# Performance work log

Measured on AMD Instinct MI355X. Metric: run time of the kernel, lower is better.

## Reference

```python
import jax, jax.numpy as jnp
import numpy as np

NFRAME = 256
NHOP = 128
BANDS = [0, 4, 8, 12, 16, 20, 24, 28, 32, 40, 44, 48, 52, 56, 64, 72, 80, 88, 96, 104, 112, 128]
NBANDS = 22


def _constants():
    F_bins = NFRAME // 2 + 1
    # sqrt-hann (periodic) analysis window
    n = np.arange(NFRAME)
    win = np.sqrt(0.5 * (1.0 - np.cos(2.0 * np.pi * n / NFRAME))).astype(np.float32)
    # triangular band filterbank matrix [NBANDS, F_bins]
    W = np.zeros((NBANDS, F_bins), np.float32)
    s, e = BANDS[0], BANDS[1]
    W[0, s:e] = 2.0 * (1.0 - np.arange(0, 1, 1.0 / (e - s)))
    s, e = BANDS[-2], BANDS[-1]
    W[-1, s:e] = 2.0 * np.arange(0, 1, 1.0 / (e - s))
    for i, (m, s, e) in enumerate(zip(BANDS[1:-1], BANDS[:-2], BANDS[2:])):
        W[i + 1, s:m] = np.arange(0, 1, 1.0 / (m - s))
        W[i + 1, m:e] = 1.0 - np.arange(0, 1, 1.0 / (e - m))
    # DCT-II matrix [NBANDS, NBANDS]
    nn = np.arange(NBANDS)
    kk = nn[:, None]
    dct = np.cos(np.pi / NBANDS * (nn + 0.5) * kk)
    dct[0] *= 1.0 / np.sqrt(2.0)
    dct *= np.sqrt(2.0 / NBANDS)
    return win, W, dct.astype(np.float32)


def setup_inputs() -> dict:
    key = jax.random.key(0)
    x = jax.random.normal(key, (32, 960000), dtype=jnp.float32)
    return {"x": x}


def reference(x):
    win, W, dct = _constants()
    B, L = x.shape
    chunks = x.reshape(B, L // NHOP, NHOP)
    frames = jnp.concatenate([chunks[:, :-1], chunks[:, 1:]], axis=-1)  # B,T,NFRAME
    frames = frames * jnp.asarray(win)
    spec = jnp.fft.rfft(frames, axis=-1)                # B,T,F complex
    pw = spec.real ** 2 + spec.imag ** 2                # |X|^2 = xk.pow(2).sum(1)
    bands_pow = jnp.einsum('btf,kf->btk', pw, jnp.asarray(W))  # fused filterbank
    feat = jnp.log10(bands_pow) @ jnp.asarray(dct).T    # B,T,22
    return feat
```

## Files before the change

### kernel.cpp

```cpp
#include <hip/hip_runtime.h>

#define NB 22
#define NFR_B 7499
#define BATCH 32
#define ROWLEN 960000
#define NFTOT (BATCH * NFR_B)

typedef float f2 __attribute__((ext_vector_type(2)));

__constant__ int c_bands[NB] = {0,4,8,12,16,20,24,28,32,40,44,48,52,56,64,72,80,88,96,104,112,128};

#define XDPP(x, CTRL) __int_as_float(__builtin_amdgcn_update_dpp(0, __float_as_int(x), CTRL, 0xF, 0xF, true))
#define XSWZ(x, PATT) __int_as_float(__builtin_amdgcn_ds_swizzle(__float_as_int(x), PATT))
#define E0S(x) XDPP(x, 0xB1)
#define E1S(x) XDPP(x, 0x4E)
#define E2S(x) XSWZ(x, 0x101F)
#define E3S(x) XDPP(x, 0x128)
#define E4S(x) XSWZ(x, 0x401F)
#define E5S(x) __shfl_xor(x, 32, 64)

__device__ __forceinline__ f2 mk2(float v) { f2 r; r.x = v; r.y = v; return r; }
__device__ __forceinline__ f2 ex0v(f2 v) { f2 r; r.x = E0S(v.x); r.y = E0S(v.y); return r; }
__device__ __forceinline__ f2 ex1v(f2 v) { f2 r; r.x = E1S(v.x); r.y = E1S(v.y); return r; }
__device__ __forceinline__ f2 ex2v(f2 v) { f2 r; r.x = E2S(v.x); r.y = E2S(v.y); return r; }
__device__ __forceinline__ f2 ex3v(f2 v) { f2 r; r.x = E3S(v.x); r.y = E3S(v.y); return r; }
__device__ __forceinline__ f2 ex4v(f2 v) { f2 r; r.x = E4S(v.x); r.y = E4S(v.y); return r; }
__device__ __forceinline__ f2 ex5v(f2 v) { f2 r; r.x = E5S(v.x); r.y = E5S(v.y); return r; }
__device__ __forceinline__ f2 shflv(f2 v, int idx) {
    f2 r; r.x = __shfl(v.x, idx, 64); r.y = __shfl(v.y, idx, 64); return r;
}

#define PSTAGE(S, EXF)                                                    \
  { const f2 exr_a = EXF(ar2), exi_a = EXF(ai2);                          \
    const f2 exr_b = EXF(br2), exi_b = EXF(bi2);                          \
    const f2 w1r = W1r[S], w1i = W1i[S], w2r = W2r[S], w2i = W2i[S];      \
    const f2 nar = w1r*ar2 - w1i*ai2 + w2r*exr_a - w2i*exi_a;             \
    const f2 nai = w1r*ai2 + w1i*ar2 + w2r*exi_a + w2i*exr_a;             \
    const f2 nbr = w1r*br2 - w1i*bi2 + w2r*exr_b - w2i*exi_b;             \
    const f2 nbi = w1r*bi2 + w1i*br2 + w2r*exi_b + w2i*exr_b;             \
    ar2 = nar; ai2 = nai; br2 = nbr; bi2 = nbi; }

__global__ __launch_bounds__(256, 3)
void feat_kernel(const float* __restrict__ x, float* __restrict__ out) {
    const int lane = threadIdx.x & 63;
    const int wid  = threadIdx.x >> 6;
    const int gwave  = blockIdx.x * (blockDim.x >> 6) + wid;
    const int nwaves = gridDim.x * (blockDim.x >> 6);

    const float PI = 3.14159265358979323846f;

    const int r = (int)(__brev((unsigned)lane) >> 25);

    float winv[4];
    #pragma unroll
    for (int j = 0; j < 4; ++j) winv[j] = sinf(PI * (float)(2 * r + j) / 256.0f);

    f2 W1r[6], W1i[6], W2r[6], W2i[6];
    #pragma unroll
    for (int s = 1; s < 6; ++s) {
        const int m = 1 << s;
        const float ang = -PI * (float)(lane & (m - 1)) / (float)m;
        const float wr = cosf(ang), wi = sinf(ang);
        const bool up = ((lane >> s) & 1) != 0;
        W1r[s] = mk2(up ? -wr : 1.0f);
        W1i[s] = mk2(up ? -wi : 0.0f);
        W2r[s] = mk2(up ? 1.0f : wr);
        W2i[s] = mk2(up ? 0.0f : wi);
    }
    const f2 sgn2 = mk2((lane & 1) ? -1.0f : 1.0f);
    const f2 w6r2 = mk2(cosf(-PI * (float)lane / 64.0f));
    const f2 w6i2 = mk2(sinf(-PI * (float)lane / 64.0f));
    const f2 c1_2 = mk2(cosf(PI * (float)lane / 128.0f));
    const f2 s1_2 = mk2(sinf(PI * (float)lane / 128.0f));

    int seg1 = 0;
    for (int j = 1; j < 14; ++j) if (lane >= c_bands[j]) seg1 = j;
    const int wd1 = c_bands[seg1 + 1] - c_bands[seg1];
    const f2 a1_2 = mk2((float)(lane - c_bands[seg1]) / (float)wd1);
    const f2 m8_2 = mk2((wd1 == 8) ? 1.0f : 0.0f);
    const int bin2 = lane + 64;
    int seg2 = 14;
    for (int j = 15; j < 21; ++j) if (bin2 >= c_bands[j]) seg2 = j;
    const int wd2 = c_bands[seg2 + 1] - c_bands[seg2];
    const f2 a2_2 = mk2((float)(bin2 - c_bands[seg2]) / (float)wd2);
    const f2 m16_2 = mk2((seg2 == 20) ? 1.0f : 0.0f);

    const int c = lane;
    int idxA = 0; bool selA1 = true;
    if (c >= 1 && c <= 21) {
        if (c - 1 <= 13) { idxA = c_bands[c - 1]; selA1 = true; }
        else             { idxA = c_bands[c - 1] - 64; selA1 = false; }
    }
    int idxD = 0; bool selD1 = true;
    if (c <= 20) {
        if (c <= 13) { idxD = c_bands[c]; selD1 = true; }
        else         { idxD = c_bands[c] - 64; selD1 = false; }
    }

    const int oc = lane & 31;
    float coef[NB];
    {
        const float norm = 0.30102999566398120f * sqrtf(2.0f / (float)NB) *
                           ((oc == 0) ? 0.70710678118654752f : 1.0f);
        #pragma unroll
        for (int b = 0; b < NB; ++b)
            coef[b] = norm * cosf(PI / (float)NB * ((float)b + 0.5f) * (float)oc);
    }
    const float accInit = (oc == 0) ? (-2.0f * 0.30102999566398120f * sqrtf(22.0f)) : 0.0f;

    const int chunk = (((NFTOT + nwaves - 1) / nwaves) + 1) & ~1;
    int f0 = gwave * chunk;
    if (f0 >= NFTOT) return;
    int f1 = f0 + chunk; if (f1 > NFTOT) f1 = NFTOT;
    const int f0u = __builtin_amdgcn_readfirstlane(f0);
    const int f1u = __builtin_amdgcn_readfirstlane(f1);

    int bb = f0u / NFR_B;
    int t0 = f0u - bb * NFR_B;
    const float* p0 = x + (size_t)bb * ROWLEN + (size_t)t0 * 128;
    int t1 = t0 + 1;
    const float* p1 = p0 + 128;
    if (t1 == NFR_B) { t1 = 0; p1 += 128; }

    float* ob = out + (size_t)f0u * NB + ((lane < 32) ? oc : (NB + oc));

    float4 v0 = *(const float4*)(p0 + 2 * r);
    float4 v1 = *(const float4*)(p1 + 2 * r);

    for (int f = f0u; f < f1u; f += 2) {
        int nt0 = t1 + 1; const float* np0 = p1 + 128;
        if (nt0 == NFR_B) { nt0 = 0; np0 += 128; }
        int nt1 = nt0 + 1; const float* np1 = np0 + 128;
        if (nt1 == NFR_B) { nt1 = 0; np1 += 128; }
        float4 nv0 = v0, nv1 = v1;
        if (f + 2 < f1u) {
            nv0 = *(const float4*)(np0 + 2 * r);
            nv1 = *(const float4*)(np1 + 2 * r);
        }

        f2 ar2 = { v0.x * winv[0], v1.x * winv[0] };
        f2 ai2 = { v0.y * winv[1], v1.y * winv[1] };
        f2 br2 = { v0.z * winv[2], v1.z * winv[2] };
        f2 bi2 = { v0.w * winv[3], v1.w * winv[3] };

        {
            const f2 e_ar = ex0v(ar2), e_ai = ex0v(ai2);
            const f2 e_br = ex0v(br2), e_bi = ex0v(bi2);
            ar2 = sgn2 * ar2 + e_ar;  ai2 = sgn2 * ai2 + e_ai;
            br2 = sgn2 * br2 + e_br;  bi2 = sgn2 * bi2 + e_bi;
        }
        PSTAGE(1, ex1v)
        PSTAGE(2, ex2v)
        PSTAGE(3, ex3v)
        PSTAGE(4, ex4v)
        PSTAGE(5, ex5v)

        {
            const f2 tr2 = w6r2 * br2 - w6i2 * bi2;
            const f2 ti2 = w6r2 * bi2 + w6i2 * br2;
            const f2 nar = ar2 + tr2, nai = ai2 + ti2;
            br2 = ar2 - tr2; bi2 = ai2 - ti2;
            ar2 = nar; ai2 = nai;
        }

        const int pidx = (64 - lane) & 63;
        const f2 par2 = shflv(ar2, pidx), pai2 = shflv(ai2, pidx);
        const f2 pbr2 = shflv(br2, pidx), pbi2 = shflv(bi2, pidx);
        const f2 P1r = (lane == 0) ? par2 : pbr2, P1i = (lane == 0) ? pai2 : pbi2;
        const f2 P2r = (lane == 0) ? pbr2 : par2, P2i = (lane == 0) ? pbi2 : pai2;

        f2 Er = ar2 + P1r, Ei = ai2 - P1i;
        f2 Or_ = ar2 - P1r, Oi = ai2 + P1i;
        const f2 X1r = Er + c1_2 * Oi - s1_2 * Or_;
        const f2 X1i = Ei - c1_2 * Or_ - s1_2 * Oi;
        const f2 pw1 = X1r * X1r + X1i * X1i;

        Er = br2 + P2r; Ei = bi2 - P2i;
        Or_ = br2 - P2r; Oi = bi2 + P2i;
        const f2 X2r = Er - s1_2 * Oi - c1_2 * Or_;
        const f2 X2i = Ei + s1_2 * Or_ - c1_2 * Oi;
        const f2 pw2 = X2r * X2r + X2i * X2i;

        f2 S1 = pw1, T1 = a1_2 * pw1;
        S1 = S1 + ex0v(S1); T1 = T1 + ex0v(T1);
        S1 = S1 + ex1v(S1); T1 = T1 + ex1v(T1);
        S1 = m8_2 * ex2v(S1) + S1; T1 = m8_2 * ex2v(T1) + T1;
        const f2 D1 = S1 - T1;
        f2 S2 = pw2, T2 = a2_2 * pw2;
        S2 = S2 + ex0v(S2); T2 = T2 + ex0v(T2);
        S2 = S2 + ex1v(S2); T2 = T2 + ex1v(T2);
        S2 = S2 + ex2v(S2); T2 = T2 + ex2v(T2);
        S2 = m16_2 * ex3v(S2) + S2; T2 = m16_2 * ex3v(T2) + T2;
        const f2 D2 = S2 - T2;

        const f2 gA1 = shflv(T1, idxA), gA2 = shflv(T2, idxA);
        const f2 gD1 = shflv(D1, idxD), gD2 = shflv(D2, idxD);
        const f2 A_prev = selA1 ? gA1 : gA2;
        const f2 D_cur  = selD1 ? gD1 : gD2;
        f2 band = A_prev + D_cur;
        if (c == 0)  band = D_cur + D_cur;
        if (c == 21) band = A_prev + A_prev;

        f2 l2;
        l2.x = __log2f(band.x);
        l2.y = __log2f(band.y);

        const float hi_sh = __shfl_xor(l2.y, 32, 64);
        const float Z = (lane < 32) ? l2.x : hi_sh;

        float acc = accInit;
        #pragma unroll
        for (int b = 0; b < NB; ++b) {
            const float zb = __shfl(Z, b, 32);
            acc = fmaf(coef[b], zb, acc);
        }
        if (oc < NB) *ob = acc;

        v0 = nv0; v1 = nv1;
        t0 = nt0; t1 = nt1; p0 = np0; p1 = np1;
        ob += 2 * NB;
    }
}

extern "C" void kernel_launch(void* const* d_in, const int* in_sizes, int n_in,
                              void* d_out, int out_size, void* d_ws, size_t ws_size,
                              hipStream_t stream) {
    const float* x = (const float*)d_in[0];
    float* out = (float*)d_out;
    feat_kernel<<<2048, 256, 0, stream>>>(x, out);
}
```

Baseline: 102.1 us.

## Cut register pressure, use DCT symmetry and bpermute for higher occupancy

Per-lane twiddle and band constants are now stored as scalars instead of duplicated float2 pairs, which reduces register usage so launch bounds can move from 3 to 7 waves per SIMD. The DCT halves its coefficient array by using cosine symmetry (coef[21-b] = ±coef[b]) and broadcasts values with ds_swizzle instead of __shfl. Shuffles are replaced with precomputed ds_bpermute addresses, and the grid size changes to 1792 blocks. The risks are added compiler spills or LDS-crossbar contention, along with a different work partition across waves.

```diff
diff --git a/kernel.cpp b/kernel.cpp
--- a/kernel.cpp
+++ b/kernel.cpp
@@ -17,30 +17,38 @@
 #define E2S(x) XSWZ(x, 0x101F)
 #define E3S(x) XDPP(x, 0x128)
 #define E4S(x) XSWZ(x, 0x401F)
-#define E5S(x) __shfl_xor(x, 32, 64)
-
+#define BC32(x, B) XSWZ(x, ((B) << 5))
+
+__device__ __forceinline__ float bperm(int addr4, float v) {
+    return __int_as_float(__builtin_amdgcn_ds_bpermute(addr4, __float_as_int(v)));
+}
 __device__ __forceinline__ f2 mk2(float v) { f2 r; r.x = v; r.y = v; return r; }
 __device__ __forceinline__ f2 ex0v(f2 v) { f2 r; r.x = E0S(v.x); r.y = E0S(v.y); return r; }
 __device__ __forceinline__ f2 ex1v(f2 v) { f2 r; r.x = E1S(v.x); r.y = E1S(v.y); return r; }
 __device__ __forceinline__ f2 ex2v(f2 v) { f2 r; r.x = E2S(v.x); r.y = E2S(v.y); return r; }
 __device__ __forceinline__ f2 ex3v(f2 v) { f2 r; r.x = E3S(v.x); r.y = E3S(v.y); return r; }
 __device__ __forceinline__ f2 ex4v(f2 v) { f2 r; r.x = E4S(v.x); r.y = E4S(v.y); return r; }
-__device__ __forceinline__ f2 ex5v(f2 v) { f2 r; r.x = E5S(v.x); r.y = E5S(v.y); return r; }
-__device__ __forceinline__ f2 shflv(f2 v, int idx) {
-    f2 r; r.x = __shfl(v.x, idx, 64); r.y = __shfl(v.y, idx, 64); return r;
+__device__ __forceinline__ f2 bpermv(int addr4, f2 v) {
+    f2 r; r.x = bperm(addr4, v.x); r.y = bperm(addr4, v.y); return r;
 }
 
 #define PSTAGE(S, EXF)                                                    \
   { const f2 exr_a = EXF(ar2), exi_a = EXF(ai2);                          \
     const f2 exr_b = EXF(br2), exi_b = EXF(bi2);                          \
-    const f2 w1r = W1r[S], w1i = W1i[S], w2r = W2r[S], w2i = W2i[S];      \
+    const f2 w1r = mk2(W1r[S]), w1i = mk2(W1i[S]);                        \
+    const f2 w2r = mk2(W2r[S]), w2i = mk2(W2i[S]);                        \
     const f2 nar = w1r*ar2 - w1i*ai2 + w2r*exr_a - w2i*exi_a;             \
     const f2 nai = w1r*ai2 + w1i*ar2 + w2r*exi_a + w2i*exr_a;             \
     const f2 nbr = w1r*br2 - w1i*bi2 + w2r*exr_b - w2i*exi_b;             \
     const f2 nbi = w1r*bi2 + w1i*br2 + w2r*exi_b + w2i*exr_b;             \
     ar2 = nar; ai2 = nai; br2 = nbr; bi2 = nbi; }
 
-__global__ __launch_bounds__(256, 3)
+#define DCTPAIR(B, ACC)                                                   \
+  { const float zlo = BC32(Z, B);                                         \
+    const float zhi = BC32(Z, 21 - (B));                                  \
+    ACC = fmaf(coef[B], fmaf(sOc, zhi, zlo), ACC); }
+
+__global__ __launch_bounds__(256, 7)
 void feat_kernel(const float* __restrict__ x, float* __restrict__ out) {
     const int lane = threadIdx.x & 63;
     const int wid  = threadIdx.x >> 6;
@@ -55,35 +63,35 @@
     #pragma unroll
     for (int j = 0; j < 4; ++j) winv[j] = sinf(PI * (float)(2 * r + j) / 256.0f);
 
-    f2 W1r[6], W1i[6], W2r[6], W2i[6];
+    float W1r[6], W1i[6], W2r[6], W2i[6];
     #pragma unroll
     for (int s = 1; s < 6; ++s) {
         const int m = 1 << s;
         const float ang = -PI * (float)(lane & (m - 1)) / (float)m;
         const float wr = cosf(ang), wi = sinf(ang);
         const bool up = ((lane >> s) & 1) != 0;
-        W1r[s] = mk2(up ? -wr : 1.0f);
-        W1i[s] = mk2(up ? -wi : 0.0f);
-        W2r[s] = mk2(up ? 1.0f : wr);
-        W2i[s] = mk2(up ? 0.0f : wi);
-    }
-    const f2 sgn2 = mk2((lane & 1) ? -1.0f : 1.0f);
-    const f2 w6r2 = mk2(cosf(-PI * (float)lane / 64.0f));
-    const f2 w6i2 = mk2(sinf(-PI * (float)lane / 64.0f));
-    const f2 c1_2 = mk2(cosf(PI * (float)lane / 128.0f));
-    const f2 s1_2 = mk2(sinf(PI * (float)lane / 128.0f));
+        W1r[s] = up ? -wr : 1.0f;
+        W1i[s] = up ? -wi : 0.0f;
+        W2r[s] = up ? 1.0f : wr;
+        W2i[s] = up ? 0.0f : wi;
+    }
+    const float sgn0 = (lane & 1) ? -1.0f : 1.0f;
+    const float w6r = cosf(-PI * (float)lane / 64.0f);
+    const float w6i = sinf(-PI * (float)lane / 64.0f);
+    const float c1 = cosf(PI * (float)lane / 128.0f);
+    const float s1 = sinf(PI * (float)lane / 128.0f);
 
     int seg1 = 0;
     for (int j = 1; j < 14; ++j) if (lane >= c_bands[j]) seg1 = j;
     const int wd1 = c_bands[seg1 + 1] - c_bands[seg1];
-    const f2 a1_2 = mk2((float)(lane - c_bands[seg1]) / (float)wd1);
-    const f2 m8_2 = mk2((wd1 == 8) ? 1.0f : 0.0f);
+    const float a1 = (float)(lane - c_bands[seg1]) / (float)wd1;
+    const float m8 = (wd1 == 8) ? 1.0f : 0.0f;
     const int bin2 = lane + 64;
     int seg2 = 14;
     for (int j = 15; j < 21; ++j) if (bin2 >= c_bands[j]) seg2 = j;
     const int wd2 = c_bands[seg2 + 1] - c_bands[seg2];
-    const f2 a2_2 = mk2((float)(bin2 - c_bands[seg2]) / (float)wd2);
-    const f2 m16_2 = mk2((seg2 == 20) ? 1.0f : 0.0f);
+    const float a2 = (float)(bin2 - c_bands[seg2]) / (float)wd2;
+    const float m16 = (seg2 == 20) ? 1.0f : 0.0f;
 
     const int c = lane;
     int idxA = 0; bool selA1 = true;
@@ -96,16 +104,21 @@
         if (c <= 13) { idxD = c_bands[c]; selD1 = true; }
         else         { idxD = c_bands[c] - 64; selD1 = false; }
     }
+    const int bpA = idxA << 2;
+    const int bpD = idxD << 2;
+    const int bpHerm = (((64 - lane) & 63) << 2);
+    const int bpX32  = ((lane ^ 32) << 2);
 
     const int oc = lane & 31;
-    float coef[NB];
+    float coef[11];
     {
         const float norm = 0.30102999566398120f * sqrtf(2.0f / (float)NB) *
                            ((oc == 0) ? 0.70710678118654752f : 1.0f);
         #pragma unroll
-        for (int b = 0; b < NB; ++b)
+        for (int b = 0; b < 11; ++b)
             coef[b] = norm * cosf(PI / (float)NB * ((float)b + 0.5f) * (float)oc);
     }
+    const float sOc = (oc & 1) ? -1.0f : 1.0f;
     const float accInit = (oc == 0) ? (-2.0f * 0.30102999566398120f * sqrtf(22.0f)) : 0.0f;
 
     const int chunk = (((NFTOT + nwaves - 1) / nwaves) + 1) & ~1;
@@ -146,55 +159,65 @@
         {
             const f2 e_ar = ex0v(ar2), e_ai = ex0v(ai2);
             const f2 e_br = ex0v(br2), e_bi = ex0v(bi2);
-            ar2 = sgn2 * ar2 + e_ar;  ai2 = sgn2 * ai2 + e_ai;
-            br2 = sgn2 * br2 + e_br;  bi2 = sgn2 * bi2 + e_bi;
+            const f2 s2 = mk2(sgn0);
+            ar2 = s2 * ar2 + e_ar;  ai2 = s2 * ai2 + e_ai;
+            br2 = s2 * br2 + e_br;  bi2 = s2 * bi2 + e_bi;
         }
         PSTAGE(1, ex1v)
         PSTAGE(2, ex2v)
         PSTAGE(3, ex3v)
         PSTAGE(4, ex4v)
-        PSTAGE(5, ex5v)
-
         {
-            const f2 tr2 = w6r2 * br2 - w6i2 * bi2;
-            const f2 ti2 = w6r2 * bi2 + w6i2 * br2;
+            const f2 exr_a = bpermv(bpX32, ar2), exi_a = bpermv(bpX32, ai2);
+            const f2 exr_b = bpermv(bpX32, br2), exi_b = bpermv(bpX32, bi2);
+            const f2 w1r = mk2(W1r[5]), w1i = mk2(W1i[5]);
+            const f2 w2r = mk2(W2r[5]), w2i = mk2(W2i[5]);
+            const f2 nar = w1r*ar2 - w1i*ai2 + w2r*exr_a - w2i*exi_a;
+            const f2 nai = w1r*ai2 + w1i*ar2 + w2r*exi_a + w2i*exr_a;
+            const f2 nbr = w1r*br2 - w1i*bi2 + w2r*exr_b - w2i*exi_b;
+            const f2 nbi = w1r*bi2 + w1i*br2 + w2r*exi_b + w2i*exr_b;
+            ar2 = nar; ai2 = nai; br2 = nbr; bi2 = nbi;
+        }
+
+        {
+            const f2 tr2 = mk2(w6r) * br2 - mk2(w6i) * bi2;
+            const f2 ti2 = mk2(w6r) * bi2 + mk2(w6i) * br2;
             const f2 nar = ar2 + tr2, nai = ai2 + ti2;
             br2 = ar2 - tr2; bi2 = ai2 - ti2;
             ar2 = nar; ai2 = nai;
         }
 
-        const int pidx = (64 - lane) & 63;
-        const f2 par2 = shflv(ar2, pidx), pai2 = shflv(ai2, pidx);
-        const f2 pbr2 = shflv(br2, pidx), pbi2 = shflv(bi2, pidx);
+        const f2 par2 = bpermv(bpHerm, ar2), pai2 = bpermv(bpHerm, ai2);
+        const f2 pbr2 = bpermv(bpHerm, br2), pbi2 = bpermv(bpHerm, bi2);
         const f2 P1r = (lane == 0) ? par2 : pbr2, P1i = (lane == 0) ? pai2 : pbi2;
         const f2 P2r = (lane == 0) ? pbr2 : par2, P2i = (lane == 0) ? pbi2 : pai2;
 
         f2 Er = ar2 + P1r, Ei = ai2 - P1i;
         f2 Or_ = ar2 - P1r, Oi = ai2 + P1i;
-        const f2 X1r = Er + c1_2 * Oi - s1_2 * Or_;
-        const f2 X1i = Ei - c1_2 * Or_ - s1_2 * Oi;
+        const f2 X1r = Er + mk2(c1) * Oi - mk2(s1) * Or_;
+        const f2 X1i = Ei - mk2(c1) * Or_ - mk2(s1) * Oi;
         const f2 pw1 = X1r * X1r + X1i * X1i;
 
         Er = br2 + P2r; Ei = bi2 - P2i;
         Or_ = br2 - P2r; Oi = bi2 + P2i;
-        const f2 X2r = Er - s1_2 * Oi - c1_2 * Or_;
-        const f2 X2i = Ei + s1_2 * Or_ - c1_2 * Oi;
+        const f2 X2r = Er - mk2(s1) * Oi - mk2(c1) * Or_;
+        const f2 X2i = Ei + mk2(s1) * Or_ - mk2(c1) * Oi;
         const f2 pw2 = X2r * X2r + X2i * X2i;
 
-        f2 S1 = pw1, T1 = a1_2 * pw1;
+        f2 S1 = pw1, T1 = mk2(a1) * pw1;
         S1 = S1 + ex0v(S1); T1 = T1 + ex0v(T1);
         S1 = S1 + ex1v(S1); T1 = T1 + ex1v(T1);
-        S1 = m8_2 * ex2v(S1) + S1; T1 = m8_2 * ex2v(T1) + T1;
+        S1 = mk2(m8) * ex2v(S1) + S1; T1 = mk2(m8) * ex2v(T1) + T1;
         const f2 D1 = S1 - T1;
-        f2 S2 = pw2, T2 = a2_2 * pw2;
+        f2 S2 = pw2, T2 = mk2(a2) * pw2;
         S2 = S2 + ex0v(S2); T2 = T2 + ex0v(T2);
         S2 = S2 + ex1v(S2); T2 = T2 + ex1v(T2);
         S2 = S2 + ex2v(S2); T2 = T2 + ex2v(T2);
-        S2 = m16_2 * ex3v(S2) + S2; T2 = m16_2 * ex3v(T2) + T2;
+        S2 = mk2(m16) * ex3v(S2) + S2; T2 = mk2(m16) * ex3v(T2) + T2;
         const f2 D2 = S2 - T2;
 
-        const f2 gA1 = shflv(T1, idxA), gA2 = shflv(T2, idxA);
-        const f2 gD1 = shflv(D1, idxD), gD2 = shflv(D2, idxD);
+        const f2 gA1 = bpermv(bpA, T1), gA2 = bpermv(bpA, T2);
+        const f2 gD1 = bpermv(bpD, D1), gD2 = bpermv(bpD, D2);
         const f2 A_prev = selA1 ? gA1 : gA2;
         const f2 D_cur  = selD1 ? gD1 : gD2;
         f2 band = A_prev + D_cur;
@@ -205,16 +228,17 @@
         l2.x = __log2f(band.x);
         l2.y = __log2f(band.y);
 
-        const float hi_sh = __shfl_xor(l2.y, 32, 64);
+        const float hi_sh = bperm(bpX32, l2.y);
         const float Z = (lane < 32) ? l2.x : hi_sh;
 
-        float acc = accInit;
-        #pragma unroll
-        for (int b = 0; b < NB; ++b) {
-            const float zb = __shfl(Z, b, 32);
-            acc = fmaf(coef[b], zb, acc);
-        }
-        if (oc < NB) *ob = acc;
+        float acc0 = accInit, acc1 = 0.0f;
+        DCTPAIR(0, acc0)  DCTPAIR(1, acc1)
+        DCTPAIR(2, acc0)  DCTPAIR(3, acc1)
+        DCTPAIR(4, acc0)  DCTPAIR(5, acc1)
+        DCTPAIR(6, acc0)  DCTPAIR(7, acc1)
+        DCTPAIR(8, acc0)  DCTPAIR(9, acc1)
+        DCTPAIR(10, acc0)
+        if (oc < NB) *ob = acc0 + acc1;
 
         v0 = nv0; v1 = nv1;
         t0 = nt0; t1 = nt1; p0 = np0; p1 = np1;
@@ -227,5 +251,5 @@
                               hipStream_t stream) {
     const float* x = (const float*)d_in[0];
     float* out = (float*)d_out;
-    feat_kernel<<<2048, 256, 0, stream>>>(x, out);
-}
+    feat_kernel<<<1792, 256, 0, stream>>>(x, out);
+}
```

After: 313.9 us. +207.4%, slower.
